# Kernel optimization log

Measured on AMD Instinct MI355X. Metric: run time of the kernel, lower is better.

## Reference

```python
import jax, jax.numpy as jnp
import numpy as np

LEAKY_SLOPE = 0.2  # self.alpha


def setup_inputs() -> dict:
    key = jax.random.key(0)
    k1, k2, k3 = jax.random.split(key, 3)
    E, F, R = 512, 256, 4
    h = jax.random.normal(k1, (E, F), dtype=jnp.float32)
    adj = jax.random.uniform(k2, (R, E, E), dtype=jnp.float32)
    lin_w = jax.random.normal(k3, (F,), dtype=jnp.float32) * (1.0 / np.sqrt(F))
    lin_b = jnp.zeros((1,), dtype=jnp.float32)
    return {"h": h, "adj": adj, "lin_w": lin_w, "lin_b": lin_b}


def reference(h, adj, lin_w, lin_b):
    # h: [E, F], adj: [R, E, E]
    adj_agg = jax.nn.softmax(jnp.sum(adj, axis=0), axis=1)          # [E, E]
    # pairwise elementwise product: a_input[i, j] = h_i * h_j
    a_input = h[:, None, :] * h[None, :, :]                          # [E, E, F]
    attention = jax.nn.leaky_relu(adj_agg[:, :, None] * a_input,
                                  negative_slope=LEAKY_SLOPE)        # [E, E, F]
    attention = jax.nn.softmax(attention, axis=0)                    # softmax over i
    # dropout p=0.0 / eval mode -> identity
    # Linear(F -> 1): scores[i, j] = attention[i, j] . w + b
    scores = jnp.einsum('ijf,f->ij', attention, lin_w) + lin_b[0]    # [E, E]
    alpha = jax.nn.softmax(jnp.sum(scores, axis=0)[None, :, None], axis=1)  # [1, E, 1]
    # h_prime[i, f] = sum_j attention[i, j, f] * h[j, f]
    h_prime = jnp.einsum('ijf,jf->if', attention, h)                 # [E, F]
    return jax.nn.elu(h_prime), alpha
```

## Files before the change

kernel.cpp:

```cpp
#include <hip/hip_runtime.h>


typedef float f2 __attribute__((ext_vector_type(2)));
typedef float f4 __attribute__((ext_vector_type(4)));

#define EE 512
#define FF 256
#define RRR 4
#define LOG2E 1.44269504088896340736f
#define TPB 512
#define RPB 4
#define NT 16
#define CH 32
#define FB 32

__global__ __launch_bounds__(256) void kA(const float* __restrict__ adj,
                                          float* __restrict__ s,
                                          float* __restrict__ out) {
    const int i = blockIdx.x;
    const int t = threadIdx.x;
    if (i == 0) {
        out[EE * FF + t]       = 1.0f / EE;
        out[EE * FF + 256 + t] = 1.0f / EE;
    }
    const float* base = adj + (size_t)i * EE;
    float t0 = 0.f, t1 = 0.f;
#pragma unroll
    for (int r = 0; r < RRR; ++r) {
        t0 += base[(size_t)r * EE * EE + t];
        t1 += base[(size_t)r * EE * EE + t + 256];
    }
    const float e0 = __expf(t0);
    const float e1 = __expf(t1);
    __shared__ float red[256];
    red[t] = e0 + e1;
    __syncthreads();
    for (int off = 128; off > 0; off >>= 1) {
        if (t < off) red[t] += red[t + off];
        __syncthreads();
    }
    const float inv = 1.0f / red[0];
    s[(size_t)i * EE + t]       = e0 * inv;
    s[(size_t)i * EE + t + 256] = e1 * inv;
}

__global__ __launch_bounds__(TPB, 8) void kB(const float* __restrict__ h,
                                             const float* __restrict__ s,
                                             f2* __restrict__ hg) {
    const int tid  = threadIdx.x;
    const int fl   = tid & (FB - 1);
    const int team = tid >> 5;
    const int j0   = blockIdx.x * RPB;
    const int f    = blockIdx.y * FB + fl;
    __shared__ __align__(16) float sl[EE * RPB];
    __shared__ float ps[NT * RPB * FB];
#pragma unroll
    for (int p = 0; p < 4; ++p) {
        const int idx = tid + p * TPB;
        sl[idx] = s[(size_t)(idx >> 2) * EE + j0 + (idx & 3)];
    }
    __syncthreads();
    const float hj0 = h[(size_t)(j0 + 0) * FF + f] * LOG2E;
    const float hj1 = h[(size_t)(j0 + 1) * FF + f] * LOG2E;
    const float hj2 = h[(size_t)(j0 + 2) * FF + f] * LOG2E;
    const float hj3 = h[(size_t)(j0 + 3) * FF + f] * LOG2E;
    const float P0 = fmaxf(hj0, 0.2f * hj0), N0 = fminf(hj0, 0.2f * hj0);
    const float P1 = fmaxf(hj1, 0.2f * hj1), N1 = fminf(hj1, 0.2f * hj1);
    const float P2 = fmaxf(hj2, 0.2f * hj2), N2 = fminf(hj2, 0.2f * hj2);
    const float P3 = fmaxf(hj3, 0.2f * hj3), N3 = fminf(hj3, 0.2f * hj3);
    float Z0 = 0.f, Z1 = 0.f, Z2 = 0.f, Z3 = 0.f;
    const float* hp = h + (size_t)(team * CH) * FF + f;
    const f4* spv = (const f4*)(sl + team * CH * RPB);
#pragma unroll 4
    for (int ii = 0; ii < CH; ++ii) {
        const float hif = hp[(size_t)ii * FF];
        const f4 sv = spv[ii];
        const bool pos = hif > 0.f;
        const float y0 = sv.x * ((pos ? P0 : N0) * hif);
        const float y1 = sv.y * ((pos ? P1 : N1) * hif);
        const float y2 = sv.z * ((pos ? P2 : N2) * hif);
        const float y3 = sv.w * ((pos ? P3 : N3) * hif);
        Z0 += __builtin_amdgcn_exp2f(y0);
        Z1 += __builtin_amdgcn_exp2f(y1);
        Z2 += __builtin_amdgcn_exp2f(y2);
        Z3 += __builtin_amdgcn_exp2f(y3);
    }
    ps[(team * RPB + 0) * FB + fl] = Z0;
    ps[(team * RPB + 1) * FB + fl] = Z1;
    ps[(team * RPB + 2) * FB + fl] = Z2;
    ps[(team * RPB + 3) * FB + fl] = Z3;
    __syncthreads();
    if (tid < RPB * FB) {
        const int r = tid >> 5, fq = tid & (FB - 1);
        float Zt = 0.f;
#pragma unroll
        for (int t = 0; t < NT; ++t) Zt += ps[(t * RPB + r) * FB + fq];
        const size_t o = (size_t)(j0 + r) * FF + blockIdx.y * FB + fq;
        const float hv = h[o];
        hg[o] = (f2){hv, hv * __builtin_amdgcn_rcpf(Zt)};
    }
}

__global__ __launch_bounds__(TPB, 8) void kC(const float* __restrict__ h,
                                             const float* __restrict__ s,
                                             const f2* __restrict__ hg,
                                             float* __restrict__ out) {
    const int tid  = threadIdx.x;
    const int fl   = tid & (FB - 1);
    const int team = tid >> 5;
    const int i0   = blockIdx.x * RPB;
    const int f    = blockIdx.y * FB + fl;
    __shared__ __align__(16) float sl[EE * RPB];
    __shared__ float ps[NT * RPB * FB];
#pragma unroll
    for (int p = 0; p < 4; ++p) {
        const int idx = tid + p * TPB;
        sl[idx] = s[(size_t)(i0 + (idx & 3)) * EE + (idx >> 2)];
    }
    __syncthreads();
    const float hl0 = h[(size_t)(i0 + 0) * FF + f] * LOG2E;
    const float hl1 = h[(size_t)(i0 + 1) * FF + f] * LOG2E;
    const float hl2 = h[(size_t)(i0 + 2) * FF + f] * LOG2E;
    const float hl3 = h[(size_t)(i0 + 3) * FF + f] * LOG2E;
    const float P0 = fmaxf(hl0, 0.2f * hl0), N0 = fminf(hl0, 0.2f * hl0);
    const float P1 = fmaxf(hl1, 0.2f * hl1), N1 = fminf(hl1, 0.2f * hl1);
    const float P2 = fmaxf(hl2, 0.2f * hl2), N2 = fminf(hl2, 0.2f * hl2);
    const float P3 = fmaxf(hl3, 0.2f * hl3), N3 = fminf(hl3, 0.2f * hl3);
    float a0 = 0.f, a1 = 0.f, a2 = 0.f, a3 = 0.f;
    const f2* hgp = hg + (size_t)(team * CH) * FF + f;
    const f4* spv = (const f4*)(sl + team * CH * RPB);
#pragma unroll 4
    for (int jj = 0; jj < CH; ++jj) {
        const f2 hgv = hgp[(size_t)jj * FF];
        const f4 sv = spv[jj];
        const bool pos = hgv.x > 0.f;
        const float y0 = sv.x * ((pos ? P0 : N0) * hgv.x);
        const float y1 = sv.y * ((pos ? P1 : N1) * hgv.x);
        const float y2 = sv.z * ((pos ? P2 : N2) * hgv.x);
        const float y3 = sv.w * ((pos ? P3 : N3) * hgv.x);
        a0 = fmaf(__builtin_amdgcn_exp2f(y0), hgv.y, a0);
        a1 = fmaf(__builtin_amdgcn_exp2f(y1), hgv.y, a1);
        a2 = fmaf(__builtin_amdgcn_exp2f(y2), hgv.y, a2);
        a3 = fmaf(__builtin_amdgcn_exp2f(y3), hgv.y, a3);
    }
    ps[(team * RPB + 0) * FB + fl] = a0;
    ps[(team * RPB + 1) * FB + fl] = a1;
    ps[(team * RPB + 2) * FB + fl] = a2;
    ps[(team * RPB + 3) * FB + fl] = a3;
    __syncthreads();
    if (tid < RPB * FB) {
        const int r = tid >> 5, fq = tid & (FB - 1);
        float a = 0.f;
#pragma unroll
        for (int t = 0; t < NT; ++t) a += ps[(t * RPB + r) * FB + fq];
        out[(size_t)(i0 + r) * FF + blockIdx.y * FB + fq] =
            (a > 0.f) ? a : (__expf(a) - 1.0f);
    }
}

extern "C" void kernel_launch(void* const* d_in, const int* in_sizes, int n_in,
                              void* d_out, int out_size, void* d_ws, size_t ws_size,
                              hipStream_t stream) {
    const float* h   = (const float*)d_in[0];
    const float* adj = (const float*)d_in[1];

    float* s   = (float*)d_ws;
    f2*    hg  = (f2*)(s + (size_t)EE * EE);
    float* out = (float*)d_out;

    kA<<<EE, 256, 0, stream>>>(adj, s, out);
    kB<<<dim3(EE / RPB, FF / FB), TPB, 0, stream>>>(h, s, hg);
    kC<<<dim3(EE / RPB, FF / FB), TPB, 0, stream>>>(h, s, hg, out);
}
```

Before: 38.02 us.

## Drop LDS staging of softmax weights, read them as wave-uniform scalar loads

Removes the shared-memory staging of the adjacency-softmax columns in kB and kC. Each wave now reads those weights straight from global memory. Team index is made wave-uniform via readfirstlane, so the weight loads can become scalar loads. The feature block widens to 64 so one wave covers one team, and blocks grow to 1024 threads. This cuts the staging loop and one barrier, at the cost of half as many blocks and possible scalar-cache latency inside the loop.

New measurement: 36.81 us, median of 2. -3.2%, faster.

```diff
diff --git a/kernel.cpp b/kernel.cpp
--- a/kernel.cpp
+++ b/kernel.cpp
@@ -2,17 +2,16 @@
 
 
 typedef float f2 __attribute__((ext_vector_type(2)));
-typedef float f4 __attribute__((ext_vector_type(4)));
 
 #define EE 512
 #define FF 256
 #define RRR 4
 #define LOG2E 1.44269504088896340736f
-#define TPB 512
+#define TPB 1024
 #define RPB 4
 #define NT 16
 #define CH 32
-#define FB 32
+#define FB 64
 
 __global__ __launch_bounds__(256) void kA(const float* __restrict__ adj,
                                           float* __restrict__ s,
@@ -47,19 +46,12 @@
 __global__ __launch_bounds__(TPB, 8) void kB(const float* __restrict__ h,
                                              const float* __restrict__ s,
                                              f2* __restrict__ hg) {
-    const int tid  = threadIdx.x;
-    const int fl   = tid & (FB - 1);
-    const int team = tid >> 5;
-    const int j0   = blockIdx.x * RPB;
-    const int f    = blockIdx.y * FB + fl;
-    __shared__ __align__(16) float sl[EE * RPB];
+    const int tid = threadIdx.x;
+    const int fl  = tid & (FB - 1);
+    const int team = __builtin_amdgcn_readfirstlane(tid >> 6);
+    const int j0  = blockIdx.x * RPB;
+    const int f   = blockIdx.y * FB + fl;
     __shared__ float ps[NT * RPB * FB];
-#pragma unroll
-    for (int p = 0; p < 4; ++p) {
-        const int idx = tid + p * TPB;
-        sl[idx] = s[(size_t)(idx >> 2) * EE + j0 + (idx & 3)];
-    }
-    __syncthreads();
     const float hj0 = h[(size_t)(j0 + 0) * FF + f] * LOG2E;
     const float hj1 = h[(size_t)(j0 + 1) * FF + f] * LOG2E;
     const float hj2 = h[(size_t)(j0 + 2) * FF + f] * LOG2E;
@@ -70,16 +62,19 @@
     const float P3 = fmaxf(hj3, 0.2f * hj3), N3 = fminf(hj3, 0.2f * hj3);
     float Z0 = 0.f, Z1 = 0.f, Z2 = 0.f, Z3 = 0.f;
     const float* hp = h + (size_t)(team * CH) * FF + f;
-    const f4* spv = (const f4*)(sl + team * CH * RPB);
+    const float* sp = s + (size_t)(team * CH) * EE + j0;
 #pragma unroll 4
     for (int ii = 0; ii < CH; ++ii) {
         const float hif = hp[(size_t)ii * FF];
-        const f4 sv = spv[ii];
+        const float s0 = sp[(size_t)ii * EE + 0];
+        const float s1 = sp[(size_t)ii * EE + 1];
+        const float s2 = sp[(size_t)ii * EE + 2];
+        const float s3 = sp[(size_t)ii * EE + 3];
         const bool pos = hif > 0.f;
-        const float y0 = sv.x * ((pos ? P0 : N0) * hif);
-        const float y1 = sv.y * ((pos ? P1 : N1) * hif);
-        const float y2 = sv.z * ((pos ? P2 : N2) * hif);
-        const float y3 = sv.w * ((pos ? P3 : N3) * hif);
+        const float y0 = s0 * ((pos ? P0 : N0) * hif);
+        const float y1 = s1 * ((pos ? P1 : N1) * hif);
+        const float y2 = s2 * ((pos ? P2 : N2) * hif);
+        const float y3 = s3 * ((pos ? P3 : N3) * hif);
         Z0 += __builtin_amdgcn_exp2f(y0);
         Z1 += __builtin_amdgcn_exp2f(y1);
         Z2 += __builtin_amdgcn_exp2f(y2);
@@ -91,7 +86,7 @@
     ps[(team * RPB + 3) * FB + fl] = Z3;
     __syncthreads();
     if (tid < RPB * FB) {
-        const int r = tid >> 5, fq = tid & (FB - 1);
+        const int r = tid >> 6, fq = tid & (FB - 1);
         float Zt = 0.f;
 #pragma unroll
         for (int t = 0; t < NT; ++t) Zt += ps[(t * RPB + r) * FB + fq];
@@ -105,19 +100,12 @@
                                              const float* __restrict__ s,
                                              const f2* __restrict__ hg,
                                              float* __restrict__ out) {
-    const int tid  = threadIdx.x;
-    const int fl   = tid & (FB - 1);
-    const int team = tid >> 5;
-    const int i0   = blockIdx.x * RPB;
-    const int f    = blockIdx.y * FB + fl;
-    __shared__ __align__(16) float sl[EE * RPB];
+    const int tid = threadIdx.x;
+    const int fl  = tid & (FB - 1);
+    const int team = __builtin_amdgcn_readfirstlane(tid >> 6);
+    const int i0  = blockIdx.x * RPB;
+    const int f   = blockIdx.y * FB + fl;
     __shared__ float ps[NT * RPB * FB];
-#pragma unroll
-    for (int p = 0; p < 4; ++p) {
-        const int idx = tid + p * TPB;
-        sl[idx] = s[(size_t)(i0 + (idx & 3)) * EE + (idx >> 2)];
-    }
-    __syncthreads();
     const float hl0 = h[(size_t)(i0 + 0) * FF + f] * LOG2E;
     const float hl1 = h[(size_t)(i0 + 1) * FF + f] * LOG2E;
     const float hl2 = h[(size_t)(i0 + 2) * FF + f] * LOG2E;
@@ -128,16 +116,19 @@
     const float P3 = fmaxf(hl3, 0.2f * hl3), N3 = fminf(hl3, 0.2f * hl3);
     float a0 = 0.f, a1 = 0.f, a2 = 0.f, a3 = 0.f;
     const f2* hgp = hg + (size_t)(team * CH) * FF + f;
-    const f4* spv = (const f4*)(sl + team * CH * RPB);
+    const float* sp = s + (size_t)i0 * EE + team * CH;
 #pragma unroll 4
     for (int jj = 0; jj < CH; ++jj) {
         const f2 hgv = hgp[(size_t)jj * FF];
-        const f4 sv = spv[jj];
+        const float s0 = sp[jj];
+        const float s1 = sp[EE + jj];
+        const float s2 = sp[2 * EE + jj];
+        const float s3 = sp[3 * EE + jj];
         const bool pos = hgv.x > 0.f;
-        const float y0 = sv.x * ((pos ? P0 : N0) * hgv.x);
-        const float y1 = sv.y * ((pos ? P1 : N1) * hgv.x);
-        const float y2 = sv.z * ((pos ? P2 : N2) * hgv.x);
-        const float y3 = sv.w * ((pos ? P3 : N3) * hgv.x);
+        const float y0 = s0 * ((pos ? P0 : N0) * hgv.x);
+        const float y1 = s1 * ((pos ? P1 : N1) * hgv.x);
+        const float y2 = s2 * ((pos ? P2 : N2) * hgv.x);
+        const float y3 = s3 * ((pos ? P3 : N3) * hgv.x);
         a0 = fmaf(__builtin_amdgcn_exp2f(y0), hgv.y, a0);
         a1 = fmaf(__builtin_amdgcn_exp2f(y1), hgv.y, a1);
         a2 = fmaf(__builtin_amdgcn_exp2f(y2), hgv.y, a2);
@@ -149,7 +140,7 @@
     ps[(team * RPB + 3) * FB + fl] = a3;
     __syncthreads();
     if (tid < RPB * FB) {
-        const int r = tid >> 5, fq = tid & (FB - 1);
+        const int r = tid >> 6, fq = tid & (FB - 1);
         float a = 0.f;
 #pragma unroll
         for (int t = 0; t < NT; ++t) a += ps[(t * RPB + r) * FB + fq];
```
